# Kernel optimization log

Measured on AMD Instinct MI355X. Metric: run time of the kernel, lower is better.

Reference implementation:

```python
import jax, jax.numpy as jnp
import numpy as np

BLOCK = 64  # hadamard_matrix_size in the torch module
IN_F, OUT_F = 2048, 2048


def _make_hadamard(size):
    m2 = np.array([[1.0, 1.0], [1.0, -1.0]], dtype=np.float32)
    m = m2
    for _ in range(int(round(np.log2(size))) - 1):
        m = np.kron(m, m2)
    return jnp.asarray(m, dtype=jnp.float32)


def block_hadamard(x, H):
    """Orthonormal Walsh-Hadamard rotation applied to blocks of size BLOCK along last dim."""
    b = H.shape[0]
    d = x.shape[-1]
    xr = x.reshape(x.shape[:-1] + (d // b, b))
    # H has +-1 entries; normalize by sqrt(b) so the rotation is orthonormal and
    # (x H)(w H)^T == x w^T exactly in real arithmetic.
    return (xr @ (H * (1.0 / jnp.sqrt(jnp.asarray(b, x.dtype))))).reshape(x.shape)


def quantize_int8(x):
    """Per-tensor symmetric int8 quantization: returns (q, scale)."""
    scale = jnp.max(jnp.abs(x)) / 127.0
    scale = jnp.maximum(scale, jnp.finfo(x.dtype).tiny)
    q = jnp.clip(jnp.round(x / scale), -127.0, 127.0)
    return q, scale


def setup_inputs() -> dict:
    key = jax.random.key(0)
    k1, k2, k3 = jax.random.split(key, 3)
    x = jax.random.normal(k1, (4, 4096, IN_F), dtype=jnp.float32)
    # kaiming_uniform-ish weight scale
    bound_w = 1.0 / np.sqrt(IN_F)
    weight = jax.random.uniform(k2, (OUT_F, IN_F), dtype=jnp.float32, minval=-bound_w, maxval=bound_w)
    bias = jax.random.uniform(k3, (OUT_F,), dtype=jnp.float32, minval=-bound_w, maxval=bound_w)
    hadamard_matrix = _make_hadamard(BLOCK)
    return {"x": x, "weight": weight, "bias": bias, "hadamard_matrix": hadamard_matrix}


def reference(x, weight, bias, hadamard_matrix):
    in_shape = x.shape
    x2 = x.reshape(-1, in_shape[-1])            # [N, in]
    x_bt = block_hadamard(x2, hadamard_matrix)   # rotated activations
    w_bt = block_hadamard(weight, hadamard_matrix)  # rotated weights (along in_features)
    x_q, x_scale = quantize_int8(x_bt)
    w_q, w_scale = quantize_int8(w_bt)
    # low-bit GEMM with inline dequant epilogue
    out = (x_q @ w_q.T) * (x_scale * w_scale)    # [N, out]
    out = out + bias
    return out.reshape(in_shape[:-1] + (weight.shape[0],))
```

## Files before the change

### kernel.cpp

```cpp
#include <hip/hip_runtime.h>
#include <cstdint>
#include <cstddef>

#define IN_F 2048
#define OUT_F 2048
#define BM 128
#define BN 128
#define BK 64

typedef int v4i __attribute__((ext_vector_type(4)));

__device__ inline void fwht64(float& a, float& b, float& c, float& d, int lane) {
    float t;
    t = a; a = t + b; b = t - b;
    t = c; c = t + d; d = t - d;
    t = a; a = t + c; c = t - c;
    t = b; b = t + d; d = t - d;
#pragma unroll
    for (int s = 1; s <= 8; s <<= 1) {
        float sg = (lane & s) ? -1.0f : 1.0f;
        float pa = __shfl_xor(a, s), pb = __shfl_xor(b, s);
        float pc = __shfl_xor(c, s), pd = __shfl_xor(d, s);
        a = fmaf(sg, a, pa);
        b = fmaf(sg, b, pb);
        c = fmaf(sg, c, pc);
        d = fmaf(sg, d, pd);
    }
}

__global__ void fwht_absmax_kernel(const float* __restrict__ in, int ngroups,
                                   float* __restrict__ partials) {
    const int lane = threadIdx.x & 63;
    const int wave = threadIdx.x >> 6;
    const int gw = (blockIdx.x * blockDim.x + threadIdx.x) >> 6;
    const int nw = (gridDim.x * blockDim.x) >> 6;
    float m = 0.0f;
    for (int g = gw; g < ngroups; g += nw) {
        float4 v = reinterpret_cast<const float4*>(in)[(size_t)g * 64 + lane];
        fwht64(v.x, v.y, v.z, v.w, lane);
        m = fmaxf(m, fmaxf(fmaxf(fabsf(v.x), fabsf(v.y)),
                           fmaxf(fabsf(v.z), fabsf(v.w))));
    }
    m *= 0.125f;
#pragma unroll
    for (int s = 32; s >= 1; s >>= 1) m = fmaxf(m, __shfl_xor(m, s));
    __shared__ float sm[4];
    if (lane == 0) sm[wave] = m;
    __syncthreads();
    if (threadIdx.x == 0)
        partials[blockIdx.x] = fmaxf(fmaxf(sm[0], sm[1]), fmaxf(sm[2], sm[3]));
}

__global__ void reduce_scales_kernel(const float* __restrict__ partX, int nX,
                                     const float* __restrict__ partW, int nW,
                                     float* __restrict__ scales) {
    const int tid = threadIdx.x;
    const int lane = tid & 63;
    const int wave = tid >> 6;
    float mx = 0.0f, mw = 0.0f;
    for (int i = tid; i < nX; i += 256) mx = fmaxf(mx, partX[i]);
    for (int i = tid; i < nW; i += 256) mw = fmaxf(mw, partW[i]);
#pragma unroll
    for (int s = 32; s >= 1; s >>= 1) {
        mx = fmaxf(mx, __shfl_xor(mx, s));
        mw = fmaxf(mw, __shfl_xor(mw, s));
    }
    __shared__ float smx[4], smw[4];
    if (lane == 0) { smx[wave] = mx; smw[wave] = mw; }
    __syncthreads();
    if (tid == 0) {
        scales[0] = fmaxf(fmaxf(smx[0], smx[1]), fmaxf(smx[2], smx[3]));
        scales[1] = fmaxf(fmaxf(smw[0], smw[1]), fmaxf(smw[2], smw[3]));
    }
}

__global__ void fwht_quant_kernel(const float* __restrict__ in, int ngroups,
                                  const float* __restrict__ amax,
                                  uint32_t* __restrict__ outq) {
    const int lane = threadIdx.x & 63;
    const int gw = (blockIdx.x * blockDim.x + threadIdx.x) >> 6;
    const int nw = (gridDim.x * blockDim.x) >> 6;
    const float scale = fmaxf(*amax / 127.0f, 1.17549435e-38f);
    const float rs = 1.0f / scale;
    for (int g = gw; g < ngroups; g += nw) {
        float4 v = reinterpret_cast<const float4*>(in)[(size_t)g * 64 + lane];
        fwht64(v.x, v.y, v.z, v.w, lane);
        float qa = fminf(fmaxf(rintf(v.x * 0.125f * rs), -127.f), 127.f);
        float qb = fminf(fmaxf(rintf(v.y * 0.125f * rs), -127.f), 127.f);
        float qc = fminf(fmaxf(rintf(v.z * 0.125f * rs), -127.f), 127.f);
        float qd = fminf(fmaxf(rintf(v.w * 0.125f * rs), -127.f), 127.f);
        uint32_t pk = ((uint32_t)((int)qa & 0xff)) |
                      ((uint32_t)((int)qb & 0xff) << 8) |
                      ((uint32_t)((int)qc & 0xff) << 16) |
                      ((uint32_t)((int)qd & 0xff) << 24);
        outq[(size_t)g * 64 + lane] = pk;
    }
}

__global__ __launch_bounds__(256, 2) void gemm_i8_kernel(
    const int8_t* __restrict__ Aq, const int8_t* __restrict__ Bq,
    const float* __restrict__ scales, const float* __restrict__ bias,
    float* __restrict__ out, int M) {
    __shared__ int8_t sA[2][BM * BK];
    __shared__ int8_t sB[2][BN * BK];
    const int tid = threadIdx.x;
    const int lane = tid & 63;
    const int wave = tid >> 6;
    const int wr = wave >> 1, wc = wave & 1;
    const int nbn = OUT_F / BN;

    int nwg = gridDim.x;
    int cpx = nwg >> 3;
    int bid = (blockIdx.x & 7) * cpx + (blockIdx.x >> 3);
    const int bm0 = (bid / nbn) * BM;
    const int bn0 = (bid % nbn) * BN;

    const int l15 = lane & 15;
    const int lseg = lane >> 4;

    const int soff0 = tid * 16;
    const int soff1 = tid * 16 + 4096;
    const int srow0 = soff0 >> 6, scol0 = soff0 & 63;
    const int srow1 = soff1 >> 6, scol1 = soff1 & 63;
    const int8_t* gA0 = Aq + (size_t)(bm0 + srow0) * IN_F + scol0;
    const int8_t* gA1 = Aq + (size_t)(bm0 + srow1) * IN_F + scol1;
    const int8_t* gB0 = Bq + (size_t)(bn0 + srow0) * IN_F + scol0;
    const int8_t* gB1 = Bq + (size_t)(bn0 + srow1) * IN_F + scol1;

#define STAGE(buf, kk)                                                                   \
    do {                                                                                 \
        __builtin_amdgcn_global_load_lds(                                                \
            (const __attribute__((address_space(1))) void*)(gA0 + (kk)),                 \
            (__attribute__((address_space(3))) void*)(&sA[buf][soff0]), 16, 0, 0);       \
        __builtin_amdgcn_global_load_lds(                                                \
            (const __attribute__((address_space(1))) void*)(gA1 + (kk)),                 \
            (__attribute__((address_space(3))) void*)(&sA[buf][soff1]), 16, 0, 0);       \
        __builtin_amdgcn_global_load_lds(                                                \
            (const __attribute__((address_space(1))) void*)(gB0 + (kk)),                 \
            (__attribute__((address_space(3))) void*)(&sB[buf][soff0]), 16, 0, 0);       \
        __builtin_amdgcn_global_load_lds(                                                \
            (const __attribute__((address_space(1))) void*)(gB1 + (kk)),                 \
            (__attribute__((address_space(3))) void*)(&sB[buf][soff1]), 16, 0, 0);       \
    } while (0)

    v4i acc[4][4] = {};

    STAGE(0, 0);
    __syncthreads();

    int cur = 0;
    for (int kk = BK; kk < IN_F; kk += BK) {
        STAGE(cur ^ 1, kk);

        v4i af[4], bf[4];
#pragma unroll
        for (int mi = 0; mi < 4; ++mi)
            af[mi] = *reinterpret_cast<const v4i*>(&sA[cur][(wr * 64 + mi * 16 + l15) * 64 + lseg * 16]);
#pragma unroll
        for (int ni = 0; ni < 4; ++ni)
            bf[ni] = *reinterpret_cast<const v4i*>(&sB[cur][(wc * 64 + ni * 16 + l15) * 64 + lseg * 16]);

#pragma unroll
        for (int mi = 0; mi < 4; ++mi)
#pragma unroll
            for (int ni = 0; ni < 4; ++ni)
                acc[mi][ni] = __builtin_amdgcn_mfma_i32_16x16x64_i8(af[mi], bf[ni], acc[mi][ni], 0, 0, 0);

        __syncthreads();
        cur ^= 1;
    }

    {
        v4i af[4], bf[4];
#pragma unroll
        for (int mi = 0; mi < 4; ++mi)
            af[mi] = *reinterpret_cast<const v4i*>(&sA[cur][(wr * 64 + mi * 16 + l15) * 64 + lseg * 16]);
#pragma unroll
        for (int ni = 0; ni < 4; ++ni)
            bf[ni] = *reinterpret_cast<const v4i*>(&sB[cur][(wc * 64 + ni * 16 + l15) * 64 + lseg * 16]);
#pragma unroll
        for (int mi = 0; mi < 4; ++mi)
#pragma unroll
            for (int ni = 0; ni < 4; ++ni)
                acc[mi][ni] = __builtin_amdgcn_mfma_i32_16x16x64_i8(af[mi], bf[ni], acc[mi][ni], 0, 0, 0);
    }
#undef STAGE

    const float sx = fmaxf(scales[0] / 127.0f, 1.17549435e-38f);
    const float sw = fmaxf(scales[1] / 127.0f, 1.17549435e-38f);
    const float f = sx * sw;

#pragma unroll
    for (int mi = 0; mi < 4; ++mi) {
#pragma unroll
        for (int ni = 0; ni < 4; ++ni) {
            const int col = bn0 + wc * 64 + ni * 16 + l15;
            const float bcol = bias[col];
#pragma unroll
            for (int r = 0; r < 4; ++r) {
                const int row = bm0 + wr * 64 + mi * 16 + lseg * 4 + r;
                out[(size_t)row * OUT_F + col] = (float)acc[mi][ni][r] * f + bcol;
            }
        }
    }
}

extern "C" void kernel_launch(void* const* d_in, const int* in_sizes, int n_in,
                              void* d_out, int out_size, void* d_ws, size_t ws_size,
                              hipStream_t stream) {
    const float* x = (const float*)d_in[0];
    const float* w = (const float*)d_in[1];
    const float* bias = (const float*)d_in[2];
    const int xN = in_sizes[0];
    const int wN = in_sizes[1];
    const int M = xN / IN_F;

    uint8_t* ws8 = (uint8_t*)d_ws;
    float* scales = (float*)ws8;
    float* partX = (float*)(ws8 + 256);
    float* partW = (float*)(ws8 + 256 + 8192);
    uint32_t* xq = (uint32_t*)(ws8 + 16384);
    uint32_t* wq = (uint32_t*)(ws8 + 16384 + (size_t)xN);

    const int xg = xN / 256;
    const int wg = wN / 256;
    const int GX = 2048, GW = 1024;
    hipLaunchKernelGGL(fwht_absmax_kernel, dim3(GX), dim3(256), 0, stream, x, xg, partX);
    hipLaunchKernelGGL(fwht_absmax_kernel, dim3(GW), dim3(256), 0, stream, w, wg, partW);
    hipLaunchKernelGGL(reduce_scales_kernel, dim3(1), dim3(256), 0, stream, partX, GX, partW, GW, scales);
    hipLaunchKernelGGL(fwht_quant_kernel, dim3(2048), dim3(256), 0, stream, x, xg, scales + 0, xq);
    hipLaunchKernelGGL(fwht_quant_kernel, dim3(1024), dim3(256), 0, stream, w, wg, scales + 1, wq);

    const int nwg = (M / BM) * (OUT_F / BN);
    hipLaunchKernelGGL(gemm_i8_kernel, dim3(nwg), dim3(256), 0, stream,
                       (const int8_t*)xq, (const int8_t*)wq, scales, bias, (float*)d_out, M);
}
```

Baseline: 356.4 us.

## Swizzle GEMM LDS tiles and merge x/w FWHT launches into single kernels

Changes the GEMM shared-memory layout so each 128-byte LDS row holds two 64-byte K-rows, with 16-byte segments XOR-swizzled by row index. The global-to-LDS loads are remapped to fill this layout, and fragment offsets are precomputed. The aim is to remove bank conflicts on the 16-byte fragment reads. It also fuses the separate x and w FWHT absmax and quant launches into single kernels that branch on block index, cutting launch count and letting the weight work overlap the activation work. The cost is extra index arithmetic and a layout that must exactly match the MFMA fragment mapping.

After: 351.8 us. Within noise of the previous version (-1.3%).

```diff
diff --git a/kernel.cpp b/kernel.cpp
--- a/kernel.cpp
+++ b/kernel.cpp
@@ -7,6 +7,8 @@
 #define BM 128
 #define BN 128
 #define BK 64
+#define GX 2048
+#define GW 1024
 
 typedef int v4i __attribute__((ext_vector_type(4)));
 
@@ -28,14 +30,20 @@
     }
 }
 
-__global__ void fwht_absmax_kernel(const float* __restrict__ in, int ngroups,
+__global__ void fwht_absmax_kernel(const float* __restrict__ xin, int xg,
+                                   const float* __restrict__ win, int wgn,
                                    float* __restrict__ partials) {
     const int lane = threadIdx.x & 63;
     const int wave = threadIdx.x >> 6;
-    const int gw = (blockIdx.x * blockDim.x + threadIdx.x) >> 6;
-    const int nw = (gridDim.x * blockDim.x) >> 6;
+    const bool isX = blockIdx.x < GX;
+    const float* __restrict__ in = isX ? xin : win;
+    const int ng = isX ? xg : wgn;
+    const int b = isX ? blockIdx.x : blockIdx.x - GX;
+    const int nblk = isX ? GX : GW;
+    const int gw = (b * blockDim.x + threadIdx.x) >> 6;
+    const int nw = (nblk * blockDim.x) >> 6;
     float m = 0.0f;
-    for (int g = gw; g < ngroups; g += nw) {
+    for (int g = gw; g < ng; g += nw) {
         float4 v = reinterpret_cast<const float4*>(in)[(size_t)g * 64 + lane];
         fwht64(v.x, v.y, v.z, v.w, lane);
         m = fmaxf(m, fmaxf(fmaxf(fabsf(v.x), fabsf(v.y)),
@@ -74,15 +82,22 @@
     }
 }
 
-__global__ void fwht_quant_kernel(const float* __restrict__ in, int ngroups,
-                                  const float* __restrict__ amax,
-                                  uint32_t* __restrict__ outq) {
+__global__ void fwht_quant_kernel(const float* __restrict__ xin, int xg,
+                                  const float* __restrict__ win, int wgn,
+                                  const float* __restrict__ scales,
+                                  uint32_t* __restrict__ xq, uint32_t* __restrict__ wq) {
     const int lane = threadIdx.x & 63;
-    const int gw = (blockIdx.x * blockDim.x + threadIdx.x) >> 6;
-    const int nw = (gridDim.x * blockDim.x) >> 6;
-    const float scale = fmaxf(*amax / 127.0f, 1.17549435e-38f);
+    const bool isX = blockIdx.x < GX;
+    const float* __restrict__ in = isX ? xin : win;
+    uint32_t* __restrict__ outq = isX ? xq : wq;
+    const int ng = isX ? xg : wgn;
+    const int b = isX ? blockIdx.x : blockIdx.x - GX;
+    const int nblk = isX ? GX : GW;
+    const int gw = (b * blockDim.x + threadIdx.x) >> 6;
+    const int nw = (nblk * blockDim.x) >> 6;
+    const float scale = fmaxf(scales[isX ? 0 : 1] / 127.0f, 1.17549435e-38f);
     const float rs = 1.0f / scale;
-    for (int g = gw; g < ngroups; g += nw) {
+    for (int g = gw; g < ng; g += nw) {
         float4 v = reinterpret_cast<const float4*>(in)[(size_t)g * 64 + lane];
         fwht64(v.x, v.y, v.z, v.w, lane);
         float qa = fminf(fmaxf(rintf(v.x * 0.125f * rs), -127.f), 127.f);
@@ -120,12 +135,14 @@
 
     const int soff0 = tid * 16;
     const int soff1 = tid * 16 + 4096;
-    const int srow0 = soff0 >> 6, scol0 = soff0 & 63;
-    const int srow1 = soff1 >> 6, scol1 = soff1 & 63;
-    const int8_t* gA0 = Aq + (size_t)(bm0 + srow0) * IN_F + scol0;
-    const int8_t* gA1 = Aq + (size_t)(bm0 + srow1) * IN_F + scol1;
-    const int8_t* gB0 = Bq + (size_t)(bn0 + srow0) * IN_F + scol0;
-    const int8_t* gB1 = Bq + (size_t)(bn0 + srow1) * IN_F + scol1;
+    int lr0 = soff0 >> 7, s0 = (soff0 >> 4) & 7, sl0 = s0 ^ (lr0 & 7);
+    int lr1 = soff1 >> 7, s1 = (soff1 >> 4) & 7, sl1 = s1 ^ (lr1 & 7);
+    const int m0 = (lr0 << 1) | (sl0 >> 2), c0 = (sl0 & 3) * 16;
+    const int m1 = (lr1 << 1) | (sl1 >> 2), c1 = (sl1 & 3) * 16;
+    const int8_t* gA0 = Aq + (size_t)(bm0 + m0) * IN_F + c0;
+    const int8_t* gA1 = Aq + (size_t)(bm0 + m1) * IN_F + c1;
+    const int8_t* gB0 = Bq + (size_t)(bn0 + m0) * IN_F + c0;
+    const int8_t* gB1 = Bq + (size_t)(bn0 + m1) * IN_F + c1;
 
 #define STAGE(buf, kk)                                                                   \
     do {                                                                                 \
@@ -143,6 +160,17 @@
             (__attribute__((address_space(3))) void*)(&sB[buf][soff1]), 16, 0, 0);       \
     } while (0)
 
+    int offA[4], offB[4];
+#pragma unroll
+    for (int mi = 0; mi < 4; ++mi) {
+        int rowA = wr * 64 + mi * 16 + l15;
+        int slA = ((rowA & 1) << 2) | lseg;
+        offA[mi] = (rowA >> 1) * 128 + (slA ^ ((rowA >> 1) & 7)) * 16;
+        int rowB = wc * 64 + mi * 16 + l15;
+        int slB = ((rowB & 1) << 2) | lseg;
+        offB[mi] = (rowB >> 1) * 128 + (slB ^ ((rowB >> 1) & 7)) * 16;
+    }
+
     v4i acc[4][4] = {};
 
     STAGE(0, 0);
@@ -155,10 +183,10 @@
         v4i af[4], bf[4];
 #pragma unroll
         for (int mi = 0; mi < 4; ++mi)
-            af[mi] = *reinterpret_cast<const v4i*>(&sA[cur][(wr * 64 + mi * 16 + l15) * 64 + lseg * 16]);
+            af[mi] = *reinterpret_cast<const v4i*>(&sA[cur][offA[mi]]);
 #pragma unroll
         for (int ni = 0; ni < 4; ++ni)
-            bf[ni] = *reinterpret_cast<const v4i*>(&sB[cur][(wc * 64 + ni * 16 + l15) * 64 + lseg * 16]);
+            bf[ni] = *reinterpret_cast<const v4i*>(&sB[cur][offB[ni]]);
 
 #pragma unroll
         for (int mi = 0; mi < 4; ++mi)
@@ -174,10 +202,10 @@
         v4i af[4], bf[4];
 #pragma unroll
         for (int mi = 0; mi < 4; ++mi)
-            af[mi] = *reinterpret_cast<const v4i*>(&sA[cur][(wr * 64 + mi * 16 + l15) * 64 + lseg * 16]);
+            af[mi] = *reinterpret_cast<const v4i*>(&sA[cur][offA[mi]]);
 #pragma unroll
         for (int ni = 0; ni < 4; ++ni)
-            bf[ni] = *reinterpret_cast<const v4i*>(&sB[cur][(wc * 64 + ni * 16 + l15) * 64 + lseg * 16]);
+            bf[ni] = *reinterpret_cast<const v4i*>(&sB[cur][offB[ni]]);
 #pragma unroll
         for (int mi = 0; mi < 4; ++mi)
 #pragma unroll
@@ -218,18 +246,18 @@
     uint8_t* ws8 = (uint8_t*)d_ws;
     float* scales = (float*)ws8;
     float* partX = (float*)(ws8 + 256);
-    float* partW = (float*)(ws8 + 256 + 8192);
+    float* partW = partX + GX;
     uint32_t* xq = (uint32_t*)(ws8 + 16384);
     uint32_t* wq = (uint32_t*)(ws8 + 16384 + (size_t)xN);
 
     const int xg = xN / 256;
     const int wg = wN / 256;
-    const int GX = 2048, GW = 1024;
-    hipLaunchKernelGGL(fwht_absmax_kernel, dim3(GX), dim3(256), 0, stream, x, xg, partX);
-    hipLaunchKernelGGL(fwht_absmax_kernel, dim3(GW), dim3(256), 0, stream, w, wg, partW);
-    hipLaunchKernelGGL(reduce_scales_kernel, dim3(1), dim3(256), 0, stream, partX, GX, partW, GW, scales);
-    hipLaunchKernelGGL(fwht_quant_kernel, dim3(2048), dim3(256), 0, stream, x, xg, scales + 0, xq);
-    hipLaunchKernelGGL(fwht_quant_kernel, dim3(1024), dim3(256), 0, stream, w, wg, scales + 1, wq);
+    hipLaunchKernelGGL(fwht_absmax_kernel, dim3(GX + GW), dim3(256), 0, stream,
+                       x, xg, w, wg, partX);
+    hipLaunchKernelGGL(reduce_scales_kernel, dim3(1), dim3(256), 0, stream,
+                       partX, GX, partW, GW, scales);
+    hipLaunchKernelGGL(fwht_quant_kernel, dim3(GX + GW), dim3(256), 0, stream,
+                       x, xg, w, wg, scales, xq, wq);
 
     const int nwg = (M / BM) * (OUT_F / BN);
     hipLaunchKernelGGL(gemm_i8_kernel, dim3(nwg), dim3(256), 0, stream,
```
